# Performance work log

Measured on AMD Instinct MI355X. Metric: run time of the kernel, lower is better.

Reference implementation:

```python
import jax, jax.numpy as jnp
import numpy as np

N, H, V, MAX_STEPS = 256, 128, 64, 4

def setup_inputs() -> dict:
    key = jax.random.key(0)
    ks = jax.random.split(key, 16)
    def w(k, shape, fan_in):
        return jax.random.normal(k, shape, dtype=jnp.float32) / np.sqrt(fan_in)
    inp = {}
    inp['node_embeddings'] = jax.random.normal(ks[0], (N, H), dtype=jnp.float32)
    inp['skip_embeddings'] = jax.random.normal(ks[1], (N, N, H), dtype=jnp.float32)
    inp['Wx'] = w(ks[2], (H, 4 * H), H)
    inp['Wh'] = w(ks[3], (H, 4 * H), H)
    inp['b'] = jnp.zeros((4 * H,), jnp.float32)
    inp['Wxs'] = w(ks[4], (H, 4 * H), H)
    inp['Whs'] = w(ks[5], (H, 4 * H), H)
    inp['bs'] = jnp.zeros((4 * H,), jnp.float32)
    inp['Wb'] = w(ks[6], (2 * H, 2), 2 * H)
    inp['bb'] = jnp.zeros((2,), jnp.float32)
    inp['Wk'] = w(ks[7], (H, H), H)
    inp['bk'] = jnp.zeros((H,), jnp.float32)
    inp['Wq'] = w(ks[8], (2 * H, H), 2 * H)
    inp['bq'] = jnp.zeros((H,), jnp.float32)
    inp['Wl'] = w(ks[9], (2 * H, 1), 2 * H)
    inp['bl'] = jnp.zeros((1,), jnp.float32)
    inp['Wd'] = w(ks[10], (2 * H, V), 2 * H)
    inp['bd'] = jnp.zeros((V,), jnp.float32)
    # valid skips only forward in the program (include diagonal = no-skip)
    inp['skip_mask'] = jnp.triu(jnp.ones((N, N), dtype=bool))
    inp['true_indexes'] = jax.random.randint(ks[11], (N,), 0, N, dtype=jnp.int32)
    inp['false_indexes'] = jax.random.randint(ks[12], (N,), 0, N, dtype=jnp.int32)
    inp['exit_index'] = N - 1
    return inp

def _lstm(c, h, x, Wx, Wh, b):
    gates = x @ Wx + h @ Wh + b  # [..., 4H]
    i, f, g, o = jnp.split(gates, 4, axis=-1)
    c2 = jax.nn.sigmoid(f) * c + jax.nn.sigmoid(i) * jnp.tanh(g)
    h2 = jax.nn.sigmoid(o) * jnp.tanh(c2)
    return c2, h2

def reference(node_embeddings, skip_embeddings, Wx, Wh, b, Wxs, Whs, bs,
              Wb, bb, Wk, bk, Wq, bq, Wl, bl, Wd, bd,
              skip_mask, true_indexes, false_indexes, exit_index):
    n, hdim = node_embeddings.shape
    eye = jnp.eye(n, dtype=node_embeddings.dtype)
    ip0 = jnp.zeros((n,), node_embeddings.dtype).at[0].set(1.0)
    c0 = jnp.zeros((n, hdim), node_embeddings.dtype)
    h0 = jnp.zeros((n, hdim), node_embeddings.dtype)
    keys = skip_embeddings @ Wk + bk  # [N,N,H] (input-only, precompute)

    def step(carry, _):
        ip, c, h = carry
        # per-node LSTM proposals
        c_p, h_p = _lstm(c, h, node_embeddings, Wx, Wh, b)  # [N,H]
        hid = jnp.concatenate([c_p, h_p], axis=-1)  # [N,2H]
        # skip proposals: carry of source i applied to skip embedding (i,j)
        c_sk, h_sk = _lstm(c[:, None, :], h[:, None, :], skip_embeddings, Wxs, Whs, bs)  # [N,N,H]
        # branch decisions
        branch = jax.nn.softmax(hid @ Wb + bb, axis=-1)  # [N,2]
        # skip decisions (per source i, softmax over destinations j)
        queries = hid @ Wq + bq  # [N,H]
        kq = jax.nn.relu(jnp.concatenate(
            [keys, jnp.broadcast_to(queries[:, None, :], (n, n, hdim))], axis=-1))  # [N,N,2H]
        logits = jnp.einsum('ijk,kl->ijl', kq, Wl)[..., 0] + bl[0]  # [N,N]
        skip_dec = jax.nn.softmax(jnp.where(skip_mask, logits, -jnp.inf), axis=-1)
        # aggregation (IPA)
        yes_skip = skip_dec * (1.0 - eye)  # zero diagonal
        no_skip = jnp.diagonal(skip_dec)
        p_bt = ip * no_skip * branch[:, 0]
        p_bf = ip * no_skip * branch[:, 1]
        new_ip = (jax.ops.segment_sum(p_bt, true_indexes, num_segments=n)
                  + jax.ops.segment_sum(p_bf, false_indexes, num_segments=n)
                  + jnp.einsum('i,ij->j', ip, yes_skip))
        denom = new_ip[:, None] + 1e-7
        def agg(hp, hsk):
            t = jax.ops.segment_sum(hp * p_bt[:, None], true_indexes, num_segments=n)
            f = jax.ops.segment_sum(hp * p_bf[:, None], false_indexes, num_segments=n)
            s = jnp.einsum('ijh,i,ij->jh', hsk, ip, yes_skip)
            return (t + f + s) / denom
        return (new_ip, agg(c_p, c_sk), agg(h_p, h_sk)), None

    (ip, c, h), _ = jax.lax.scan(step, (ip0, c0, h0), None, length=MAX_STEPS)
    exit_concat = jnp.concatenate([c[exit_index], h[exit_index]], axis=-1)  # [2H]
    return exit_concat @ Wd + bd  # [V]
```

## Files before the change

### kernel.cpp

```cpp
#include <hip/hip_runtime.h>
#include <hip/hip_bf16.h>

constexpr int NN = 256;
constexpr int HH = 128;
constexpr int GG = 512;
constexpr int NP = NN * NN;

typedef __attribute__((ext_vector_type(8))) short short8;
typedef __attribute__((ext_vector_type(4))) float f32x4;

__device__ unsigned short g_xs[(size_t)NP * GG];
__device__ unsigned short g_wpk[5 * 128 * 128];
__device__ float g_bsp[GG];
__device__ float g_pwh[HH * HH * 4];
__device__ float g_pws[HH * HH * 4];
__device__ float g_kterm[NP];
__device__ float g_yesw[NP];
__device__ float g_noskip[NN];
__device__ float g_xg[NN * GG];
__device__ float g_hws[NN * HH * 4];
__device__ float g_c[NN * HH];
__device__ float g_h[NN * HH];
__device__ float g_sc[NN * HH];
__device__ float g_sh[NN * HH];
__device__ float g_ip[NN];
__device__ float g_nip[NN];

__device__ __forceinline__ unsigned short f2bf(float f) {
  unsigned int u = __float_as_uint(f);
  u = (u + 0x7fffu + ((u >> 16) & 1u)) >> 16;
  return (unsigned short)u;
}
__device__ __forceinline__ float bf2f(unsigned short s) {
  return __uint_as_float(((unsigned int)s) << 16);
}
__device__ __forceinline__ float frcp(float x) {
#if __has_builtin(__builtin_amdgcn_rcpf)
  return __builtin_amdgcn_rcpf(x);
#else
  return 1.0f / x;
#endif
}
__device__ __forceinline__ float sigm(float x) { return frcp(1.f + __expf(-x)); }
__device__ __forceinline__ float tanhfast(float x) { return 1.f - 2.f * frcp(__expf(2.f * x) + 1.f); }

__global__ void k_init() {
  int idx = blockIdx.x * blockDim.x + threadIdx.x;
  g_sc[idx] = 0.f; g_sh[idx] = 0.f; g_c[idx] = 0.f; g_h[idx] = 0.f;
  *(float4*)&g_hws[(size_t)idx * 4] = make_float4(0.f, 0.f, 0.f, 0.f);
  if (idx < NN) { g_nip[idx] = 0.f; g_ip[idx] = (idx == 0) ? 1.f : 0.f; }
}

__global__ __launch_bounds__(128) void k_prep(const float* __restrict__ Wxs,
                                              const float* __restrict__ Wk,
                                              const float* __restrict__ bs) {
  const int tile = blockIdx.x;
  const int c = blockIdx.y;
  const int k = threadIdx.x;
  float v;
  if (tile < 4) {
    const int src = (c & 3) * 128 + tile * 32 + (c >> 2);
    v = Wxs[k * GG + src];
    if (k == 0) g_bsp[tile * 128 + c] = bs[src];
  } else {
    v = Wk[k * HH + c];
  }
  char* base = (char*)g_wpk + tile * 32768;
  *(unsigned short*)(base + c * 256 + ((k * 2) ^ ((c & 7) << 4))) = f2bf(v);
}

__global__ __launch_bounds__(128) void k_prep2(const float* __restrict__ Wh,
                                               const float* __restrict__ Whs) {
  const int k = blockIdx.x, t = threadIdx.x;
  float4 a = make_float4(Wh[k * GG + t], Wh[k * GG + 128 + t], Wh[k * GG + 256 + t], Wh[k * GG + 384 + t]);
  float4 s = make_float4(Whs[k * GG + t], Whs[k * GG + 128 + t], Whs[k * GG + 256 + t], Whs[k * GG + 384 + t]);
  *(float4*)&g_pwh[((size_t)k * HH + t) * 4] = a;
  *(float4*)&g_pws[((size_t)k * HH + t) * 4] = s;
}

__global__ __launch_bounds__(128) void k_xg(const float* __restrict__ NE,
                                            const float* __restrict__ Wx,
                                            const float* __restrict__ b) {
  const int i = blockIdx.x, t = threadIdx.x;
  __shared__ float ne[HH];
  ne[t] = NE[i * HH + t];
  __syncthreads();
  float a0 = b[t], a1 = b[128 + t], a2 = b[256 + t], a3 = b[384 + t];
  for (int k = 0; k < HH; ++k) {
    float x = ne[k];
    a0 = fmaf(x, Wx[k * GG + t], a0);
    a1 = fmaf(x, Wx[k * GG + 128 + t], a1);
    a2 = fmaf(x, Wx[k * GG + 256 + t], a2);
    a3 = fmaf(x, Wx[k * GG + 384 + t], a3);
  }
  g_xg[i * GG + t] = a0; g_xg[i * GG + 128 + t] = a1;
  g_xg[i * GG + 256 + t] = a2; g_xg[i * GG + 384 + t] = a3;
}

__global__ __launch_bounds__(256) void k_gemm(const float* __restrict__ SE,
                                              const float* __restrict__ bk,
                                              const float* __restrict__ Wl) {
  __shared__ __align__(16) char lds[65536];
  const int pb = blockIdx.x;
  const int i_row = pb >> 1;
  const int jlo = (pb & 1) * 128;
  if (jlo + 127 < i_row) return;
  const int pairBase = pb * 128;
  const int tid = threadIdx.x;

  for (int cc = tid; cc < 2048; cc += 256) {
    int row = cc >> 4, kc = cc & 15;
    const float* src = SE + (size_t)(pairBase + row) * HH + kc * 8;
    float4 f0 = *(const float4*)(src);
    float4 f1 = *(const float4*)(src + 4);
    short8 v;
    v[0] = (short)f2bf(f0.x); v[1] = (short)f2bf(f0.y); v[2] = (short)f2bf(f0.z); v[3] = (short)f2bf(f0.w);
    v[4] = (short)f2bf(f1.x); v[5] = (short)f2bf(f1.y); v[6] = (short)f2bf(f1.z); v[7] = (short)f2bf(f1.w);
    *(short8*)(lds + row * 256 + ((kc * 16) ^ ((row & 7) << 4))) = v;
  }
  __syncthreads();

  const int wv = tid >> 6;
  const int l = tid & 63;
  const int l15 = l & 15, lg = l >> 4;

  short8 afr[4][2];
#pragma unroll
  for (int ks = 0; ks < 4; ++ks) {
    const int kb = ks * 64 + lg * 16;
#pragma unroll
    for (int rt = 0; rt < 2; ++rt) {
      int row = wv * 32 + rt * 16 + l15;
      afr[ks][rt] = *(const short8*)(lds + row * 256 + (kb ^ ((row & 7) << 4)));
    }
  }

  for (int tile = 0; tile < 5; ++tile) {
    __syncthreads();
    {
      const char* src = (const char*)g_wpk + tile * 32768;
#pragma unroll
      for (int it = 0; it < 8; ++it) {
        int off = it * 4096 + tid * 16;
        *(short8*)(lds + 32768 + off) = *(const short8*)(src + off);
      }
    }
    __syncthreads();

    f32x4 acc[2][8];
#pragma unroll
    for (int rt = 0; rt < 2; ++rt)
#pragma unroll
      for (int ct = 0; ct < 8; ++ct) acc[rt][ct] = (f32x4){0.f, 0.f, 0.f, 0.f};

#pragma unroll
    for (int ks = 0; ks < 4; ++ks) {
      const int kb = ks * 64 + lg * 16;
      short8 bfr[8];
#pragma unroll
      for (int ct = 0; ct < 8; ++ct) {
        int col = ct * 16 + l15;
        bfr[ct] = *(const short8*)(lds + 32768 + col * 256 + (kb ^ ((col & 7) << 4)));
      }
#pragma unroll
      for (int rt = 0; rt < 2; ++rt)
#pragma unroll
        for (int ct = 0; ct < 8; ++ct)
          acc[rt][ct] = __builtin_amdgcn_mfma_f32_16x16x32_bf16(afr[ks][rt], bfr[ct], acc[rt][ct], 0, 0, 0);
    }

    if (tile < 4) {
#pragma unroll
      for (int rt = 0; rt < 2; ++rt)
#pragma unroll
        for (int ct = 0; ct < 8; ++ct) {
          const int col = ct * 16 + l15;
          const float bsv = g_bsp[tile * 128 + col];
#pragma unroll
          for (int r = 0; r < 4; ++r) {
            int row = wv * 32 + rt * 16 + lg * 4 + r;
            int pair = pairBase + row;
            int jj = pair & 255, ii = pair >> 8;
            if (jj > ii) g_xs[(size_t)pair * GG + tile * 128 + col] = f2bf(acc[rt][ct][r] + bsv);
          }
        }
    } else {
#pragma unroll
      for (int rt = 0; rt < 2; ++rt) {
#pragma unroll
        for (int r = 0; r < 4; ++r) {
          float s = 0.f;
#pragma unroll
          for (int ct = 0; ct < 8; ++ct) {
            int col = ct * 16 + l15;
            float x = acc[rt][ct][r] + bk[col];
            x = fmaxf(x, 0.f);
            s = fmaf(x, Wl[col], s);
          }
#pragma unroll
          for (int m = 1; m < 16; m <<= 1) s += __shfl_xor(s, m, 64);
          int row = wv * 32 + rt * 16 + lg * 4 + r;
          int pair = pairBase + row;
          int jj = pair & 255, ii = pair >> 8;
          if (l15 == 0 && jj >= ii) g_kterm[pair] = s;
        }
      }
    }
  }
}

__global__ __launch_bounds__(256) void k_softmax() {
  const int i = blockIdx.x, j = threadIdx.x;
  __shared__ float sm[NN];
  float x = -1e30f;
  if (j >= i) x = g_kterm[i * NN + j];
  sm[j] = x;
  __syncthreads();
  for (int s = 128; s > 0; s >>= 1) { if (j < s) sm[j] = fmaxf(sm[j], sm[j + s]); __syncthreads(); }
  float mx = sm[0];
  __syncthreads();
  float e = (j >= i) ? __expf(x - mx) : 0.f;
  sm[j] = e;
  __syncthreads();
  for (int s = 128; s > 0; s >>= 1) { if (j < s) sm[j] += sm[j + s]; __syncthreads(); }
  float p = e * frcp(sm[0]);
  g_yesw[i * NN + j] = (j == i) ? 0.f : p;
  if (j == i) g_noskip[i] = p;
}

__global__ __launch_bounds__(128) void k_step(const float* __restrict__ Wb,
                                              const float* __restrict__ bb,
                                              const int* __restrict__ tix,
                                              const int* __restrict__ fix) {
  const int t = threadIdx.x;
  __shared__ float hsm[HH];
  __shared__ float red[2][2];
  if (blockIdx.x < 256) {
    const int i = blockIdx.x;
    hsm[t] = g_h[i * HH + t];
    __syncthreads();
    float a0 = g_xg[i * GG + t], a1 = g_xg[i * GG + 128 + t];
    float a2 = g_xg[i * GG + 256 + t], a3 = g_xg[i * GG + 384 + t];
    for (int k = 0; k < HH; ++k) {
      float hv = hsm[k];
      const float4 wa = *(const float4*)&g_pwh[((size_t)k * HH + t) * 4];
      a0 = fmaf(hv, wa.x, a0); a1 = fmaf(hv, wa.y, a1);
      a2 = fmaf(hv, wa.z, a2); a3 = fmaf(hv, wa.w, a3);
    }
    float co = g_c[i * HH + t];
    float c2 = sigm(a1) * co + sigm(a0) * tanhfast(a2);
    float h2 = sigm(a3) * tanhfast(c2);
    float q0 = c2 * Wb[2 * t] + h2 * Wb[2 * (128 + t)];
    float q1 = c2 * Wb[2 * t + 1] + h2 * Wb[2 * (128 + t) + 1];
#pragma unroll
    for (int m = 1; m < 64; m <<= 1) { q0 += __shfl_xor(q0, m, 64); q1 += __shfl_xor(q1, m, 64); }
    if ((t & 63) == 0) { red[t >> 6][0] = q0; red[t >> 6][1] = q1; }
    __syncthreads();
    float l0 = red[0][0] + red[1][0] + bb[0];
    float l1 = red[0][1] + red[1][1] + bb[1];
    float mm = fmaxf(l0, l1);
    float e0 = __expf(l0 - mm), e1 = __expf(l1 - mm);
    float inv = frcp(e0 + e1);
    float ipv = g_ip[i] * g_noskip[i];
    if (ipv != 0.f) {
      float pbt = ipv * e0 * inv, pbf = ipv * e1 * inv;
      int ti = tix[i], fi = fix[i];
      atomicAdd(&g_sc[ti * HH + t], c2 * pbt);
      atomicAdd(&g_sh[ti * HH + t], h2 * pbt);
      atomicAdd(&g_sc[fi * HH + t], c2 * pbf);
      atomicAdd(&g_sh[fi * HH + t], h2 * pbf);
      if (t == 0) { atomicAdd(&g_nip[ti], pbt); atomicAdd(&g_nip[fi], pbf); }
    }
  } else {
    const int idx = blockIdx.x - 256;
    const int j = idx >> 3, chunk = idx & 7;
    const int i0 = chunk * 32;
    if (i0 >= j) return;
    const int i1 = (i0 + 32 < j) ? (i0 + 32) : j;
    float accC = 0.f, accH = 0.f, accW = 0.f;
    for (int i = i0; i < i1; ++i) {
      float wgt = g_ip[i] * g_yesw[i * NN + j];
      if (wgt == 0.f) continue;
      const ushort4 gv = *(const ushort4*)&g_xs[((size_t)(i * NN + j) * 128 + t) * 4];
      float4 hw = *(const float4*)&g_hws[((size_t)i * HH + t) * 4];
      float xi = bf2f(gv.x) + hw.x;
      float xf = bf2f(gv.y) + hw.y;
      float xg = bf2f(gv.z) + hw.z;
      float xo = bf2f(gv.w) + hw.w;
      float c2 = sigm(xf) * g_c[i * HH + t] + sigm(xi) * tanhfast(xg);
      float h2 = sigm(xo) * tanhfast(c2);
      accC = fmaf(wgt, c2, accC);
      accH = fmaf(wgt, h2, accH);
      accW += wgt;
    }
    if (accW != 0.f) {
      atomicAdd(&g_sc[j * HH + t], accC);
      atomicAdd(&g_sh[j * HH + t], accH);
      if (t == 0) atomicAdd(&g_nip[j], accW);
    }
  }
}

__global__ __launch_bounds__(128) void k_finish() {
  const int j = blockIdx.x, t = threadIdx.x;
  __shared__ float hsm[HH];
  float nip = g_nip[j];
  float d = frcp(nip + 1e-7f);
  float cv = g_sc[j * HH + t] * d;
  float hv = g_sh[j * HH + t] * d;
  g_c[j * HH + t] = cv;
  g_h[j * HH + t] = hv;
  hsm[t] = hv;
  g_sc[j * HH + t] = 0.f;
  g_sh[j * HH + t] = 0.f;
  if (t == 0) { g_ip[j] = nip; g_nip[j] = 0.f; }
  __syncthreads();
  float s0 = 0.f, s1 = 0.f, s2 = 0.f, s3 = 0.f;
  for (int k = 0; k < HH; ++k) {
    float hk = hsm[k];
    const float4 w = *(const float4*)&g_pws[((size_t)k * HH + t) * 4];
    s0 = fmaf(hk, w.x, s0); s1 = fmaf(hk, w.y, s1);
    s2 = fmaf(hk, w.z, s2); s3 = fmaf(hk, w.w, s3);
  }
  *(float4*)&g_hws[((size_t)j * HH + t) * 4] = make_float4(s0, s1, s2, s3);
}

__global__ __launch_bounds__(64) void k_out(const float* __restrict__ Wd,
                                            const float* __restrict__ bd,
                                            const int* __restrict__ ei,
                                            float* __restrict__ out) {
  const int v = threadIdx.x;
  const int e = ei[0];
  float s = bd[v];
  for (int h = 0; h < HH; ++h) {
    s = fmaf(g_c[e * HH + h], Wd[h * 64 + v], s);
    s = fmaf(g_h[e * HH + h], Wd[(128 + h) * 64 + v], s);
  }
  out[v] = s;
}

extern "C" void kernel_launch(void* const* d_in, const int* in_sizes, int n_in,
                              void* d_out, int out_size, void* d_ws, size_t ws_size,
                              hipStream_t stream) {
  const float* NE  = (const float*)d_in[0];
  const float* SE  = (const float*)d_in[1];
  const float* Wx  = (const float*)d_in[2];
  const float* Wh  = (const float*)d_in[3];
  const float* b   = (const float*)d_in[4];
  const float* Wxs = (const float*)d_in[5];
  const float* Whs = (const float*)d_in[6];
  const float* bs  = (const float*)d_in[7];
  const float* Wb  = (const float*)d_in[8];
  const float* bb  = (const float*)d_in[9];
  const float* Wk  = (const float*)d_in[10];
  const float* bk  = (const float*)d_in[11];
  const float* Wl  = (const float*)d_in[14];
  const float* Wd  = (const float*)d_in[16];
  const float* bd  = (const float*)d_in[17];
  const int* tix = (const int*)d_in[19];
  const int* fix = (const int*)d_in[20];
  const int* ei  = (const int*)d_in[21];
  float* out = (float*)d_out;

  k_init<<<256, 128, 0, stream>>>();
  k_prep<<<dim3(5, 128), 128, 0, stream>>>(Wxs, Wk, bs);
  k_prep2<<<128, 128, 0, stream>>>(Wh, Whs);
  k_xg<<<256, 128, 0, stream>>>(NE, Wx, b);
  k_gemm<<<512, 256, 0, stream>>>(SE, bk, Wl);
  k_softmax<<<256, 256, 0, stream>>>();
  for (int s = 0; s < 4; ++s) {
    k_step<<<256 + 2048, 128, 0, stream>>>(Wb, bb, tix, fix);
    k_finish<<<256, 128, 0, stream>>>();
  }
  k_out<<<1, 64, 0, stream>>>(Wd, bd, ei, out);
}
```

Measured before the change: 181.1 us.

## Prepack MFMA B fragments in global, trim GEMM grid, split step and finish work

Weights are now prepacked into per-lane MFMA fragment order in global memory. The GEMM reads B fragments straight from global/L2 with double buffering instead of staging them through LDS, which halves LDS use and removes block syncs. The GEMM grid is compacted to launch only the 384 blocks that do useful work, skipping the early-exit ones. The step kernel uses finer 16-row chunks with weights cached in shared memory, and finish splits its 128-wide matvec across two halves and skips it on the last step. The trade-off is more global loads per wave in the GEMM and more atomics from the finer chunking.

```diff
diff --git a/kernel.cpp b/kernel.cpp
--- a/kernel.cpp
+++ b/kernel.cpp
@@ -10,7 +10,7 @@
 typedef __attribute__((ext_vector_type(4))) float f32x4;
 
 __device__ unsigned short g_xs[(size_t)NP * GG];
-__device__ unsigned short g_wpk[5 * 128 * 128];
+__device__ unsigned short g_wfr[20 * 512 * 8];
 __device__ float g_bsp[GG];
 __device__ float g_pwh[HH * HH * 4];
 __device__ float g_pws[HH * HH * 4];
@@ -51,22 +51,25 @@
   if (idx < NN) { g_nip[idx] = 0.f; g_ip[idx] = (idx == 0) ? 1.f : 0.f; }
 }
 
-__global__ __launch_bounds__(128) void k_prep(const float* __restrict__ Wxs,
+__global__ __launch_bounds__(512) void k_prep(const float* __restrict__ Wxs,
                                               const float* __restrict__ Wk,
                                               const float* __restrict__ bs) {
-  const int tile = blockIdx.x;
-  const int c = blockIdx.y;
-  const int k = threadIdx.x;
-  float v;
-  if (tile < 4) {
-    const int src = (c & 3) * 128 + tile * 32 + (c >> 2);
-    v = Wxs[k * GG + src];
-    if (k == 0) g_bsp[tile * 128 + c] = bs[src];
-  } else {
-    v = Wk[k * HH + c];
-  }
-  char* base = (char*)g_wpk + tile * 32768;
-  *(unsigned short*)(base + c * 256 + ((k * 2) ^ ((c & 7) << 4))) = f2bf(v);
+  const int bidx = blockIdx.x;
+  const int tile = bidx >> 2, ks = bidx & 3;
+  const int s = threadIdx.x;
+  const int ct = s >> 6, l = s & 63;
+  const int c = ct * 16 + (l & 15);
+  const int kbase = ks * 32 + (l >> 4) * 8;
+  int src = 0;
+  if (tile < 4) src = (c & 3) * 128 + tile * 32 + (c >> 2);
+  unsigned short* dst = &g_wfr[((size_t)bidx * 512 + s) * 8];
+#pragma unroll
+  for (int e = 0; e < 8; ++e) {
+    int k = kbase + e;
+    float v = (tile < 4) ? Wxs[k * GG + src] : Wk[k * HH + c];
+    dst[e] = f2bf(v);
+  }
+  if (tile < 4 && ks == 0 && (l >> 4) == 0) g_bsp[tile * 128 + c] = bs[src];
 }
 
 __global__ __launch_bounds__(128) void k_prep2(const float* __restrict__ Wh,
@@ -97,14 +100,18 @@
   g_xg[i * GG + 256 + t] = a2; g_xg[i * GG + 384 + t] = a3;
 }
 
+__device__ __forceinline__ void loadB(short8* dst, int tile, int ks, int l) {
+  const unsigned short* wf = &g_wfr[((size_t)(tile * 4 + ks)) * 4096 + l * 8];
+#pragma unroll
+  for (int ct = 0; ct < 8; ++ct) dst[ct] = *(const short8*)(wf + ct * 512);
+}
+
 __global__ __launch_bounds__(256) void k_gemm(const float* __restrict__ SE,
                                               const float* __restrict__ bk,
                                               const float* __restrict__ Wl) {
-  __shared__ __align__(16) char lds[65536];
-  const int pb = blockIdx.x;
-  const int i_row = pb >> 1;
-  const int jlo = (pb & 1) * 128;
-  if (jlo + 127 < i_row) return;
+  __shared__ __align__(16) char lds[32768];
+  const int bid = blockIdx.x;
+  const int pb = (bid < 128) ? (bid * 2) : ((bid - 128) * 2 + 1);
   const int pairBase = pb * 128;
   const int tid = threadIdx.x;
 
@@ -124,49 +131,48 @@
   const int l = tid & 63;
   const int l15 = l & 15, lg = l >> 4;
 
-  short8 afr[4][2];
-#pragma unroll
-  for (int ks = 0; ks < 4; ++ks) {
-    const int kb = ks * 64 + lg * 16;
-#pragma unroll
-    for (int rt = 0; rt < 2; ++rt) {
-      int row = wv * 32 + rt * 16 + l15;
-      afr[ks][rt] = *(const short8*)(lds + row * 256 + (kb ^ ((row & 7) << 4)));
-    }
-  }
-
+#pragma unroll 1
   for (int tile = 0; tile < 5; ++tile) {
-    __syncthreads();
-    {
-      const char* src = (const char*)g_wpk + tile * 32768;
-#pragma unroll
-      for (int it = 0; it < 8; ++it) {
-        int off = it * 4096 + tid * 16;
-        *(short8*)(lds + 32768 + off) = *(const short8*)(src + off);
+    f32x4 acc[2][8];
+#pragma unroll
+    for (int rt = 0; rt < 2; ++rt)
+#pragma unroll
+      for (int ct = 0; ct < 8; ++ct) acc[rt][ct] = (f32x4){0.f, 0.f, 0.f, 0.f};
+
+    short8 bA[8], bB[8];
+    loadB(bA, tile, 0, l);
+#pragma unroll
+    for (int ks = 0; ks < 4; ks += 2) {
+      loadB(bB, tile, ks + 1, l);
+      {
+        const int kb = ks * 64 + lg * 16;
+        short8 a[2];
+#pragma unroll
+        for (int rt = 0; rt < 2; ++rt) {
+          int row = wv * 32 + rt * 16 + l15;
+          a[rt] = *(const short8*)(lds + row * 256 + (kb ^ ((row & 7) << 4)));
+        }
+#pragma unroll
+        for (int rt = 0; rt < 2; ++rt)
+#pragma unroll
+          for (int ct = 0; ct < 8; ++ct)
+            acc[rt][ct] = __builtin_amdgcn_mfma_f32_16x16x32_bf16(a[rt], bA[ct], acc[rt][ct], 0, 0, 0);
       }
-    }
-    __syncthreads();
-
-    f32x4 acc[2][8];
-#pragma unroll
-    for (int rt = 0; rt < 2; ++rt)
-#pragma unroll
-      for (int ct = 0; ct < 8; ++ct) acc[rt][ct] = (f32x4){0.f, 0.f, 0.f, 0.f};
-
-#pragma unroll
-    for (int ks = 0; ks < 4; ++ks) {
-      const int kb = ks * 64 + lg * 16;
-      short8 bfr[8];
-#pragma unroll
-      for (int ct = 0; ct < 8; ++ct) {
-        int col = ct * 16 + l15;
-        bfr[ct] = *(const short8*)(lds + 32768 + col * 256 + (kb ^ ((col & 7) << 4)));
+      if (ks + 2 < 4) loadB(bA, tile, ks + 2, l);
+      {
+        const int kb = (ks + 1) * 64 + lg * 16;
+        short8 a[2];
+#pragma unroll
+        for (int rt = 0; rt < 2; ++rt) {
+          int row = wv * 32 + rt * 16 + l15;
+          a[rt] = *(const short8*)(lds + row * 256 + (kb ^ ((row & 7) << 4)));
+        }
+#pragma unroll
+        for (int rt = 0; rt < 2; ++rt)
+#pragma unroll
+          for (int ct = 0; ct < 8; ++ct)
+            acc[rt][ct] = __builtin_amdgcn_mfma_f32_16x16x32_bf16(a[rt], bB[ct], acc[rt][ct], 0, 0, 0);
       }
-#pragma unroll
-      for (int rt = 0; rt < 2; ++rt)
-#pragma unroll
-        for (int ct = 0; ct < 8; ++ct)
-          acc[rt][ct] = __builtin_amdgcn_mfma_f32_16x16x32_bf16(afr[ks][rt], bfr[ct], acc[rt][ct], 0, 0, 0);
     }
 
     if (tile < 4) {
@@ -233,10 +239,10 @@
                                               const int* __restrict__ tix,
                                               const int* __restrict__ fix) {
   const int t = threadIdx.x;
-  __shared__ float hsm[HH];
-  __shared__ float red[2][2];
   if (blockIdx.x < 256) {
     const int i = blockIdx.x;
+    __shared__ float hsm[HH];
+    __shared__ float red[2][2];
     hsm[t] = g_h[i * HH + t];
     __syncthreads();
     float a0 = g_xg[i * GG + t], a1 = g_xg[i * GG + 128 + t];
@@ -273,14 +279,18 @@
     }
   } else {
     const int idx = blockIdx.x - 256;
-    const int j = idx >> 3, chunk = idx & 7;
-    const int i0 = chunk * 32;
+    const int j = idx >> 4, chunk = idx & 15;
+    const int i0 = chunk * 16;
     if (i0 >= j) return;
-    const int i1 = (i0 + 32 < j) ? (i0 + 32) : j;
+    const int iN = (j - i0 < 16) ? (j - i0) : 16;
+    __shared__ float wsh[16];
+    if (t < 16) wsh[t] = (t < iN) ? g_ip[i0 + t] * g_yesw[(i0 + t) * NN + j] : 0.f;
+    __syncthreads();
     float accC = 0.f, accH = 0.f, accW = 0.f;
-    for (int i = i0; i < i1; ++i) {
-      float wgt = g_ip[i] * g_yesw[i * NN + j];
+    for (int ii = 0; ii < iN; ++ii) {
+      float wgt = wsh[ii];
       if (wgt == 0.f) continue;
+      const int i = i0 + ii;
       const ushort4 gv = *(const ushort4*)&g_xs[((size_t)(i * NN + j) * 128 + t) * 4];
       float4 hw = *(const float4*)&g_hws[((size_t)i * HH + t) * 4];
       float xi = bf2f(gv.x) + hw.x;
@@ -301,28 +311,40 @@
   }
 }
 
-__global__ __launch_bounds__(128) void k_finish() {
-  const int j = blockIdx.x, t = threadIdx.x;
+__global__ __launch_bounds__(256) void k_finish(const int last) {
+  const int j = blockIdx.x, tid = threadIdx.x;
+  const int t = tid & 127, half = tid >> 7;
   __shared__ float hsm[HH];
-  float nip = g_nip[j];
-  float d = frcp(nip + 1e-7f);
-  float cv = g_sc[j * HH + t] * d;
-  float hv = g_sh[j * HH + t] * d;
-  g_c[j * HH + t] = cv;
-  g_h[j * HH + t] = hv;
-  hsm[t] = hv;
-  g_sc[j * HH + t] = 0.f;
-  g_sh[j * HH + t] = 0.f;
-  if (t == 0) { g_ip[j] = nip; g_nip[j] = 0.f; }
-  __syncthreads();
+  __shared__ float4 part[2][HH];
+  if (half == 0) {
+    float nip = g_nip[j];
+    float d = frcp(nip + 1e-7f);
+    float cv = g_sc[j * HH + t] * d;
+    float hv = g_sh[j * HH + t] * d;
+    g_c[j * HH + t] = cv;
+    g_h[j * HH + t] = hv;
+    hsm[t] = hv;
+    g_sc[j * HH + t] = 0.f;
+    g_sh[j * HH + t] = 0.f;
+    if (t == 0) { g_ip[j] = nip; g_nip[j] = 0.f; }
+  }
+  __syncthreads();
+  if (last) return;
   float s0 = 0.f, s1 = 0.f, s2 = 0.f, s3 = 0.f;
-  for (int k = 0; k < HH; ++k) {
+  const int k0 = half * 64;
+  for (int k = k0; k < k0 + 64; ++k) {
     float hk = hsm[k];
     const float4 w = *(const float4*)&g_pws[((size_t)k * HH + t) * 4];
     s0 = fmaf(hk, w.x, s0); s1 = fmaf(hk, w.y, s1);
     s2 = fmaf(hk, w.z, s2); s3 = fmaf(hk, w.w, s3);
   }
-  *(float4*)&g_hws[((size_t)j * HH + t) * 4] = make_float4(s0, s1, s2, s3);
+  part[half][t] = make_float4(s0, s1, s2, s3);
+  __syncthreads();
+  if (half == 0) {
+    float4 a = part[0][t], bq = part[1][t];
+    *(float4*)&g_hws[((size_t)j * HH + t) * 4] =
+        make_float4(a.x + bq.x, a.y + bq.y, a.z + bq.z, a.w + bq.w);
+  }
 }
 
 __global__ __launch_bounds__(64) void k_out(const float* __restrict__ Wd,
@@ -363,14 +385,14 @@
   float* out = (float*)d_out;
 
   k_init<<<256, 128, 0, stream>>>();
-  k_prep<<<dim3(5, 128), 128, 0, stream>>>(Wxs, Wk, bs);
+  k_prep<<<20, 512, 0, stream>>>(Wxs, Wk, bs);
   k_prep2<<<128, 128, 0, stream>>>(Wh, Whs);
   k_xg<<<256, 128, 0, stream>>>(NE, Wx, b);
-  k_gemm<<<512, 256, 0, stream>>>(SE, bk, Wl);
+  k_gemm<<<384, 256, 0, stream>>>(SE, bk, Wl);
   k_softmax<<<256, 256, 0, stream>>>();
   for (int s = 0; s < 4; ++s) {
-    k_step<<<256 + 2048, 128, 0, stream>>>(Wb, bb, tix, fix);
-    k_finish<<<256, 128, 0, stream>>>();
+    k_step<<<256 + 4096, 128, 0, stream>>>(Wb, bb, tix, fix);
+    k_finish<<<256, 256, 0, stream>>>(s == 3);
   }
   k_out<<<1, 64, 0, stream>>>(Wd, bd, ei, out);
 }
```

Result: faster. 165.7 us (-8.5%).
